# Kernel tuning notes

Measured on AMD Instinct MI355X. Metric: run time of the kernel, lower is better.

Reference implementation:

```python
import jax, jax.numpy as jnp
import numpy as np

B, S, H = 2, 2048, 2048
NH, NKV, HD = 16, 4, 128
ROPE_BASE = 10000.0


def setup_inputs() -> dict:
    key = jax.random.key(0)
    ks = jax.random.split(key, 5)
    x = jax.random.normal(ks[0], (B, S, H), dtype=jnp.float32)
    position_ids = jnp.arange(S, dtype=jnp.int64 if jax.config.jax_enable_x64 else jnp.int32).reshape(1, S)
    # Linear weights stored as [in, out] (equivalent to torch weight.T)
    sc = 1.0 / np.sqrt(H)
    Wq = jax.random.normal(ks[1], (H, NH * HD), dtype=jnp.float32) * sc
    Wk = jax.random.normal(ks[2], (H, NKV * HD), dtype=jnp.float32) * sc
    Wv = jax.random.normal(ks[3], (H, NKV * HD), dtype=jnp.float32) * sc
    Wo = jax.random.normal(ks[4], (NH * HD, H), dtype=jnp.float32) * (1.0 / np.sqrt(NH * HD))
    return {"x": x, "position_ids": position_ids, "Wq": Wq, "Wk": Wk, "Wv": Wv, "Wo": Wo}


def _rope(q, k, position_ids):
    # q: [B,S,NH,HD], k: [B,S,NKV,HD]; Llama-style half-split RoPE
    half = HD // 2
    inv_freq = 1.0 / (ROPE_BASE ** (jnp.arange(0, half, dtype=jnp.float32) * 2.0 / HD))
    ang = position_ids.astype(jnp.float32)[..., None] * inv_freq  # [b,S,half]
    cos = jnp.concatenate([jnp.cos(ang), jnp.cos(ang)], axis=-1)[:, :, None, :]  # [b,S,1,HD]
    sin = jnp.concatenate([jnp.sin(ang), jnp.sin(ang)], axis=-1)[:, :, None, :]

    def rot_half(t):
        t1, t2 = t[..., :half], t[..., half:]
        return jnp.concatenate([-t2, t1], axis=-1)

    return q * cos + rot_half(q) * sin, k * cos + rot_half(k) * sin


def reference(x, position_ids, Wq, Wk, Wv, Wo):
    b, s, _ = x.shape
    q = (x @ Wq).reshape(b, s, NH, HD)
    k = (x @ Wk).reshape(b, s, NKV, HD)
    v = (x @ Wv).reshape(b, s, NKV, HD)
    q, k = _rope(q, k, position_ids)
    reps = NH // NKV
    k = jnp.repeat(k, reps, axis=2)  # repeat_interleave on head dim
    v = jnp.repeat(v, reps, axis=2)
    q = q.transpose(0, 2, 1, 3)  # [b,h,s,d]
    k = k.transpose(0, 2, 1, 3)
    v = v.transpose(0, 2, 1, 3)
    scores = jnp.einsum('bhqd,bhkd->bhqk', q, k) / jnp.sqrt(jnp.float32(HD))
    causal = jnp.triu(jnp.ones((s, s), dtype=bool), k=1)
    scores = jnp.where(causal, -jnp.inf, scores)
    attn = jax.nn.softmax(scores.astype(jnp.float32), axis=-1).astype(q.dtype)
    out = jnp.einsum('bhqk,bhkd->bhqd', attn, v)
    out = out.transpose(0, 2, 1, 3).reshape(b, s, NH * HD)
    return out @ Wo
```

## Files before the change

kernel.cpp:

```cpp
#include <hip/hip_runtime.h>
#include <stdint.h>

typedef unsigned short u16;
typedef __attribute__((ext_vector_type(8))) short short8;
typedef __attribute__((ext_vector_type(4))) short short4v;
typedef __attribute__((ext_vector_type(4))) float floatx4;

#define S_LEN 2048
#define NQKV 3072

#if __has_builtin(__builtin_amdgcn_exp2f)
#define EXP2F __builtin_amdgcn_exp2f
#else
#define EXP2F exp2f
#endif

__device__ inline float bf2f(u16 u) {
  union { uint32_t u; float f; } v; v.u = ((uint32_t)u) << 16; return v.f;
}
__device__ inline u16 f2bf(float f) {
  union { float f; uint32_t u; } v; v.f = f;
  uint32_t r = v.u + 0x7fffu + ((v.u >> 16) & 1u);
  return (u16)(r >> 16);
}
__device__ inline void gl2lds16(const u16* g, u16* l) {
  __builtin_amdgcn_global_load_lds((const __attribute__((address_space(1))) uint32_t*)g,
                                   (__attribute__((address_space(3))) uint32_t*)l, 16, 0, 0);
}

__global__ void prep_k(const float* __restrict__ x, u16* __restrict__ Xb,
                       const float* __restrict__ Wq, const float* __restrict__ Wk,
                       const float* __restrict__ Wv, const float* __restrict__ Wo,
                       u16* __restrict__ WT, u16* __restrict__ WoT,
                       const int* __restrict__ pos, float2* __restrict__ rtab) {
  __shared__ u16 tile[64][33];
  const int b = blockIdx.x, t = threadIdx.x;
  if (b < 8192) {
    int i = b * 256 + t;
    float4 v = ((const float4*)x)[i];
    ushort4 o;
    o.x = f2bf(v.x); o.y = f2bf(v.y); o.z = f2bf(v.z); o.w = f2bf(v.w);
    ((ushort4*)Xb)[i] = o;
    return;
  }
  if (b >= 13312) {
    int i = (b - 13312) * 256 + t;
    int s = i >> 6, d = i & 63;
    float freq = __expf(-(float)d * 0.015625f * 9.210340371976184f);
    float ang = (float)pos[s] * freq;
    rtab[i] = make_float2(cosf(ang), sinf(ang));
    return;
  }
  int wb = b - 8192;
  const float* src; u16* dst; int bx, by, N;
  if (wb < 2048)      { src = Wq; dst = WT;                       bx = wb & 63;          by = wb >> 6;          N = 2048; }
  else if (wb < 2560) { src = Wk; dst = WT + (size_t)2048 * 2048; bx = (wb - 2048) & 15; by = (wb - 2048) >> 4; N = 512;  }
  else if (wb < 3072) { src = Wv; dst = WT + (size_t)2560 * 2048; bx = (wb - 2560) & 15; by = (wb - 2560) >> 4; N = 512;  }
  else                { src = Wo; dst = WoT;                      bx = (wb - 3072) & 63; by = (wb - 3072) >> 6; N = 2048; }
  int n0 = bx * 32, k0 = by * 64;
  int tx = t & 31, ty = t >> 5;
#pragma unroll
  for (int i = 0; i < 8; i++)
    tile[ty + 8 * i][tx] = f2bf(src[(size_t)(k0 + ty + 8 * i) * N + n0 + tx]);
  __syncthreads();
  int n = t >> 3, kc = (t & 7) * 8;
  short8 v;
#pragma unroll
  for (int j = 0; j < 8; j++) v[j] = (short)tile[kc + j][n];
  *(short8*)(dst + (size_t)(n0 + n) * 2048 + k0 + kc) = v;
}

__global__ __launch_bounds__(256) void gemm128_k(const u16* __restrict__ A,
                                                 const u16* __restrict__ Bt,
                                                 float* __restrict__ C, int M, int N, int K) {
  __shared__ u16 Al[2][8192];
  __shared__ u16 Bl[2][8192];
  const int TN = N >> 7;
  int flat = blockIdx.x;
  const int cpx = gridDim.x >> 3;
  flat = (flat & 7) * cpx + (flat >> 3);
  const int m0 = (flat / TN) << 7, n0 = (flat % TN) << 7;
  const int t = threadIdx.x, w = t >> 6, lane = t & 63;
  const int quad = lane >> 4, l16 = lane & 15;
  const int wm = w >> 1, wn = w & 1;
  const int sr = t >> 3, sl = t & 7;
  floatx4 acc[4][4] = {};
  const int NKT = K >> 6;
  const int ra_l = wm * 64 + l16;
  const int rb_l = wn * 64 + l16;

#pragma unroll
  for (int round = 0; round < 4; round++) {
    int r = round * 32 + sr;
    int so = (sl ^ (r & 7)) << 3;
    gl2lds16(A + (size_t)(m0 + r) * K + so, &Al[0][0] + round * 2048 + t * 8);
    gl2lds16(Bt + (size_t)(n0 + r) * K + so, &Bl[0][0] + round * 2048 + t * 8);
  }
  asm volatile("s_waitcnt vmcnt(0)" ::: "memory");
  __builtin_amdgcn_s_barrier();

  for (int kt = 0; kt < NKT; kt++) {
    const int cur = kt & 1;
    __builtin_amdgcn_s_barrier();
    if (kt + 1 < NKT) {
      const int k1 = (kt + 1) << 6;
#pragma unroll
      for (int round = 0; round < 4; round++) {
        int r = round * 32 + sr;
        int so = (sl ^ (r & 7)) << 3;
        gl2lds16(A + (size_t)(m0 + r) * K + k1 + so, &Al[cur ^ 1][0] + round * 2048 + t * 8);
        gl2lds16(Bt + (size_t)(n0 + r) * K + k1 + so, &Bl[cur ^ 1][0] + round * 2048 + t * 8);
      }
      asm volatile("s_waitcnt vmcnt(8)" ::: "memory");
    } else {
      asm volatile("s_waitcnt vmcnt(0)" ::: "memory");
    }
    __builtin_amdgcn_s_barrier();
    const u16* Ab = &Al[cur][0];
    const u16* Bb = &Bl[cur][0];
    short8 af[4][2], bf[4][2];
#pragma unroll
    for (int mt = 0; mt < 4; mt++) {
      int ra = ra_l + mt * 16;
      const u16* base = Ab + ra * 64;
#pragma unroll
      for (int ks = 0; ks < 2; ks++)
        af[mt][ks] = *(const short8*)(base + (((ks * 4 + quad) ^ (ra & 7)) << 3));
    }
#pragma unroll
    for (int nt = 0; nt < 4; nt++) {
      int rb = rb_l + nt * 16;
      const u16* base = Bb + rb * 64;
#pragma unroll
      for (int ks = 0; ks < 2; ks++)
        bf[nt][ks] = *(const short8*)(base + (((ks * 4 + quad) ^ (rb & 7)) << 3));
    }
    __builtin_amdgcn_s_setprio(1);
#pragma unroll
    for (int mt = 0; mt < 4; mt++)
#pragma unroll
      for (int nt = 0; nt < 4; nt++)
#pragma unroll
        for (int ks = 0; ks < 2; ks++)
          acc[mt][nt] = __builtin_amdgcn_mfma_f32_16x16x32_bf16(af[mt][ks], bf[nt][ks], acc[mt][nt], 0, 0, 0);
    __builtin_amdgcn_s_setprio(0);
  }
#pragma unroll
  for (int mt = 0; mt < 4; mt++)
#pragma unroll
    for (int nt = 0; nt < 4; nt++)
#pragma unroll
      for (int r = 0; r < 4; r++) {
        int row = m0 + wm * 64 + mt * 16 + quad * 4 + r;
        int col = n0 + wn * 64 + nt * 16 + l16;
        C[(size_t)row * N + col] = acc[mt][nt][r];
      }
}

__global__ __launch_bounds__(512, 2) void gemm256_k(const u16* __restrict__ A,
                                                    const u16* __restrict__ Bt,
                                                    u16* __restrict__ C,
                                                    const float2* __restrict__ rtab,
                                                    int N, int K) {
  __shared__ u16 SM[65536];
  u16* const AlB = SM;
  u16* const BlB = SM + 32768;
  const int TN = N >> 8;
  int flat = blockIdx.x;
  const int cpx = gridDim.x >> 3;
  flat = (flat & 7) * cpx + (flat >> 3);
  const int m0 = (flat / TN) << 8, n0 = (flat % TN) << 8;
  const int t = threadIdx.x, w = t >> 6, lane = t & 63;
  const int quad = lane >> 4, l16 = lane & 15;
  const int wm = w >> 2, wn = w & 3;
  const int sr = t >> 3, sl = t & 7;
  floatx4 acc[2][2][4][2] = {};
  const int NKT = K >> 6;

  const int ra_l = wm * 64 + l16;
  const int rb_l = wn * 16 + l16;

#pragma unroll
  for (int round = 0; round < 2; round++) {
    int r = round * 64 + sr;
    int so = (sl ^ (r & 7)) << 3;
    gl2lds16(A + (size_t)(m0 + r) * K + so, AlB + round * 4096 + t * 8);
    gl2lds16(Bt + (size_t)(n0 + r) * K + so, BlB + round * 4096 + t * 8);
    gl2lds16(Bt + (size_t)(n0 + 128 + r) * K + so, BlB + 8192 + round * 4096 + t * 8);
    gl2lds16(A + (size_t)(m0 + 128 + r) * K + so, AlB + 8192 + round * 4096 + t * 8);
  }
  asm volatile("s_waitcnt vmcnt(0)" ::: "memory");
  __builtin_amdgcn_s_barrier();

  short8 af[4][2];
  short8 bf[2][2][2];

  for (int kt = 0; kt < NKT; kt++) {
    const int c = kt & 1;
    const u16* Ab = AlB + c * 16384;
    const u16* Bb = BlB + c * 16384;
    u16* An = AlB + (c ^ 1) * 16384;
    u16* Bn = BlB + (c ^ 1) * 16384;
    const int k1 = (kt + 1) << 6;
    const bool pf = (kt + 1 < NKT);
#pragma unroll
    for (int ph = 0; ph < 4; ph++) {
      const int mh = (ph >> 1);
      const int nh = (ph == 1 || ph == 2) ? 1 : 0;
      if (ph == 0 || ph == 1) {
#pragma unroll
        for (int nt = 0; nt < 2; nt++) {
          int rb = rb_l + nt * 64;
          const u16* base = Bb + nh * 8192 + rb * 64;
#pragma unroll
          for (int ks = 0; ks < 2; ks++)
            bf[nh][nt][ks] = *(const short8*)(base + (((ks * 4 + quad) ^ (rb & 7)) << 3));
        }
      }
      if (ph == 0 || ph == 2) {
#pragma unroll
        for (int mt = 0; mt < 4; mt++) {
          int ra = ra_l + mt * 16;
          const u16* base = Ab + mh * 8192 + ra * 64;
#pragma unroll
          for (int ks = 0; ks < 2; ks++)
            af[mt][ks] = *(const short8*)(base + (((ks * 4 + quad) ^ (ra & 7)) << 3));
        }
      }
      if (pf) {
        const u16* G;
        u16* L;
        int rbase;
        if (ph == 0)      { G = A;  L = An;        rbase = m0; }
        else if (ph == 1) { G = Bt; L = Bn;        rbase = n0; }
        else if (ph == 2) { G = Bt; L = Bn + 8192; rbase = n0 + 128; }
        else              { G = A;  L = An + 8192; rbase = m0 + 128; }
#pragma unroll
        for (int round = 0; round < 2; round++) {
          int r = round * 64 + sr;
          gl2lds16(G + (size_t)(rbase + r) * K + k1 + ((sl ^ (r & 7)) << 3),
                   L + round * 4096 + t * 8);
        }
      }
      __builtin_amdgcn_s_barrier();
      __builtin_amdgcn_s_setprio(1);
#pragma unroll
      for (int mt = 0; mt < 4; mt++)
#pragma unroll
        for (int nt = 0; nt < 2; nt++)
#pragma unroll
          for (int ks = 0; ks < 2; ks++)
            acc[mh][nh][mt][nt] =
                __builtin_amdgcn_mfma_f32_16x16x32_bf16(af[mt][ks], bf[nh][nt][ks], acc[mh][nh][mt][nt], 0, 0, 0);
      __builtin_amdgcn_s_setprio(0);
      if (ph != 2) {
        if (pf) asm volatile("s_waitcnt vmcnt(4)" ::: "memory");
        else    asm volatile("s_waitcnt vmcnt(0)" ::: "memory");
      }
      __builtin_amdgcn_s_barrier();
    }
  }
  if (n0 < 2560) {
    const int dloc = wn * 16 + l16;
#pragma unroll
    for (int mh = 0; mh < 2; mh++)
#pragma unroll
      for (int mt = 0; mt < 4; mt++)
#pragma unroll
        for (int r = 0; r < 4; r++) {
          int row = m0 + mh * 128 + wm * 64 + mt * 16 + quad * 4 + r;
          float2 cs = rtab[(row & (S_LEN - 1)) * 64 + dloc];
#pragma unroll
          for (int nh = 0; nh < 2; nh++) {
            float a0 = acc[mh][nh][mt][0][r], a1 = acc[mh][nh][mt][1][r];
            float o0 = a0 * cs.x - a1 * cs.y;
            float o1 = a1 * cs.x + a0 * cs.y;
            int colb = n0 + nh * 128 + wn * 16 + l16;
            C[(size_t)row * N + colb]      = f2bf(o0);
            C[(size_t)row * N + colb + 64] = f2bf(o1);
          }
        }
  } else {
    const int bbv = m0 >> 11, m0loc = m0 & 2047;
    const int kvbase = (n0 - 2560) >> 7;
#pragma unroll
    for (int mh = 0; mh < 2; mh++)
#pragma unroll
      for (int nh = 0; nh < 2; nh++)
#pragma unroll
        for (int mt = 0; mt < 4; mt++)
#pragma unroll
          for (int pair = 0; pair < 2; pair++) {
            int lrow = mh * 128 + wm * 64 + mt * 16 + quad * 4;
            int lcol = nh * 128 + wn * 16 + l16 + pair * 64;
            short4v v4 = { (short)f2bf(acc[mh][nh][mt][pair][0]),
                           (short)f2bf(acc[mh][nh][mt][pair][1]),
                           (short)f2bf(acc[mh][nh][mt][pair][2]),
                           (short)f2bf(acc[mh][nh][mt][pair][3]) };
            *(short4v*)(SM + lcol * 256 + (lrow ^ ((lcol & 15) << 3))) = v4;
          }
    asm volatile("s_waitcnt lgkmcnt(0)" ::: "memory");
    __builtin_amdgcn_s_barrier();
#pragma unroll
    for (int it = 0; it < 16; it++) {
      int u = it * 512 + t;
      int key0 = (u & 31) * 8, lcol = u >> 5;
      short8 v = *(const short8*)(SM + lcol * 256 + (key0 ^ ((lcol & 15) << 3)));
      int d = lcol & 127, kvh = kvbase + (lcol >> 7);
      int key = m0loc + key0;
      *(short8*)(C + (size_t)(bbv * 2048 + kvh * 512 + d * 4 + (key >> 9)) * N + 2560 + (key & 511)) = v;
    }
  }
}

__global__ __launch_bounds__(256) void attn_k(const u16* __restrict__ qkv,
                                              u16* __restrict__ ctx) {
  __shared__ u16 Kl[2][64 * 128];
  __shared__ u16 Vl[2][128 * 64];
  const int f = blockIdx.x;
  const int p = f >> 5;
  const int hb = f & 31;
  const int h = hb & 15, bb = hb >> 4;
  const int kvh = h >> 2;
  const int t = threadIdx.x, w = t >> 6, lane = t & 63;
  const int quad = lane >> 4, l16 = lane & 15;
  const int sx = l16 & 7;
  const int kslot = lane & 15;
  const int vd0 = w * 32 + (lane >> 3);
  const int vslot = lane & 7;
  const int grow0 = (w & 1) * 4 + (w >> 1) * 32 + quad;
  const size_t rowbase = (size_t)bb * S_LEN;
  const u16* Kg0 = qkv + rowbase * NQKV + 2048 + kvh * 128;
  const u16* Vg0 = qkv + (rowbase + kvh * 512) * NQKV + 2560;
  const float c2 = 0.12751744f;
  short8 onesf = {16256, 16256, 16256, 16256, 16256, 16256, 16256, 16256};

  for (int phase = 0; phase < 2; phase++) {
    const int qt = phase ? p : 31 - p;
    const int rw = qt * 64 + w * 16;
    const int qrow = rw + l16;

    short8 qf[4];
#pragma unroll
    for (int ks = 0; ks < 4; ks++)
      qf[ks] = *(const short8*)(qkv + (rowbase + rw + l16) * NQKV + h * 128 + ks * 32 + quad * 8);

    floatx4 acc[8] = {};
    floatx4 accl = {0.f, 0.f, 0.f, 0.f};

    __syncthreads();
    {
#pragma unroll
      for (int ii = 0; ii < 4; ii++) {
        int p7 = (quad + 4 * ii) & 7;
        int grow = grow0 + 8 * ii;
        gl2lds16(Kg0 + (size_t)grow * NQKV + ((kslot ^ p7) * 8),
                 &Kl[0][0] + w * 2048 + ii * 512 + lane * 8);
      }
#pragma unroll
      for (int ii = 0; ii < 4; ii++) {
        int d = vd0 + ii * 8;
        int s8 = (vslot ^ (d & 7)) * 8;
        gl2lds16(Vg0 + (size_t)(d * 4) * NQKV + s8,
                 &Vl[0][0] + w * 2048 + ii * 512 + lane * 8);
      }
    }

    for (int kb = 0; kb <= qt; kb++) {
      const int cur = kb & 1;
      __builtin_amdgcn_s_barrier();
      if (kb < qt) {
        const int kn = kb + 1;
        const u16* Kg = Kg0 + (size_t)kn * 64 * NQKV;
        u16* KlN = &Kl[cur ^ 1][0];
        u16* VlN = &Vl[cur ^ 1][0];
#pragma unroll
        for (int ii = 0; ii < 4; ii++) {
          int p7 = (quad + 4 * ii) & 7;
          int grow = grow0 + 8 * ii;
          gl2lds16(Kg + (size_t)grow * NQKV + ((kslot ^ p7) * 8),
                   KlN + w * 2048 + ii * 512 + lane * 8);
        }
#pragma unroll
        for (int ii = 0; ii < 4; ii++) {
          int d = vd0 + ii * 8;
          int s8 = (vslot ^ (d & 7)) * 8;
          gl2lds16(Vg0 + (size_t)(d * 4 + (kn >> 3)) * NQKV + (kn & 7) * 64 + s8,
                   VlN + w * 2048 + ii * 512 + lane * 8);
        }
        asm volatile("s_waitcnt vmcnt(8)" ::: "memory");
      } else {
        asm volatile("s_waitcnt vmcnt(0)" ::: "memory");
      }
      __builtin_amdgcn_s_barrier();
      const u16* KlB = &Kl[cur][0];
      const u16* VlB = &Vl[cur][0];

      floatx4 sc[4];
      __builtin_amdgcn_s_setprio(1);
#pragma unroll
      for (int nt = 0; nt < 4; nt++) {
        const u16* Krow = KlB + (nt * 16 + l16) * 128;
        short8 kf[4];
#pragma unroll
        for (int ks = 0; ks < 4; ks++)
          kf[ks] = *(const short8*)(Krow + (((ks * 4 + quad) ^ sx) * 8));
        floatx4 s = {0.f, 0.f, 0.f, 0.f};
#pragma unroll
        for (int ks = 0; ks < 4; ks++) s = __builtin_amdgcn_mfma_f32_16x16x32_bf16(kf[ks], qf[ks], s, 0, 0, 0);
        sc[nt] = s;
      }
      __builtin_amdgcn_s_setprio(0);
      const bool diag = (kb == qt);
      uint32_t pw[8];
#pragma unroll
      for (int nt = 0; nt < 4; nt++) {
        uint32_t w0 = 0, w1 = 0;
#pragma unroll
        for (int r = 0; r < 4; r++) {
          float e = EXP2F(sc[nt][r] * c2);
          if (diag) {
            int keyg = kb * 64 + quad * 8 + (nt & 1) * 4 + (nt >> 1) * 32 + r;
            if (keyg > qrow) e = 0.f;
          }
          uint32_t b = __float_as_uint(e) >> 16;
          if (r == 0) w0 = b;
          else if (r == 1) w0 |= b << 16;
          else if (r == 2) w1 = b;
          else w1 |= b << 16;
        }
        pw[nt * 2] = w0;
        pw[nt * 2 + 1] = w1;
      }
      union { short8 v; uint32_t u[4]; } pu0, pu1;
      pu0.u[0] = pw[0]; pu0.u[1] = pw[1]; pu0.u[2] = pw[2]; pu0.u[3] = pw[3];
      pu1.u[0] = pw[4]; pu1.u[1] = pw[5]; pu1.u[2] = pw[6]; pu1.u[3] = pw[7];
      const short8 pf0 = pu0.v, pf1 = pu1.v;

      __builtin_amdgcn_s_setprio(1);
      accl = __builtin_amdgcn_mfma_f32_16x16x32_bf16(pf0, onesf, accl, 0, 0, 0);
      accl = __builtin_amdgcn_mfma_f32_16x16x32_bf16(pf1, onesf, accl, 0, 0, 0);
#pragma unroll
      for (int nto = 0; nto < 8; nto++) {
        const u16* Vrow = VlB + (nto * 16 + l16) * 64;
        short8 vf0 = *(const short8*)(Vrow + ((quad ^ sx) * 8));
        short8 vf1 = *(const short8*)(Vrow + (((quad + 4) ^ sx) * 8));
        acc[nto] = __builtin_amdgcn_mfma_f32_16x16x32_bf16(pf0, vf0, acc[nto], 0, 0, 0);
        acc[nto] = __builtin_amdgcn_mfma_f32_16x16x32_bf16(pf1, vf1, acc[nto], 0, 0, 0);
      }
      __builtin_amdgcn_s_setprio(0);
    }
#pragma unroll
    for (int r = 0; r < 4; r++) {
      float inv = 1.0f / accl[r];
      int rowg = rw + quad * 4 + r;
#pragma unroll
      for (int nto = 0; nto < 8; nto++) {
        int col = h * 128 + nto * 16 + l16;
        ctx[(rowbase + rowg) * 2048 + col] = f2bf(acc[nto][r] * inv);
      }
    }
  }
}

extern "C" void kernel_launch(void* const* d_in, const int* in_sizes, int n_in,
                              void* d_out, int out_size, void* d_ws, size_t ws_size,
                              hipStream_t stream) {
  const float* x  = (const float*)d_in[0];
  const int* pos  = (const int*)d_in[1];
  const float* Wq = (const float*)d_in[2];
  const float* Wk = (const float*)d_in[3];
  const float* Wv = (const float*)d_in[4];
  const float* Wo = (const float*)d_in[5];
  float* out = (float*)d_out;
  char* ws = (char*)d_ws;
  u16* Xb  = (u16*)(ws);
  u16* WT  = (u16*)(ws + 16777216);
  u16* WoT = (u16*)(ws + 29360128);
  u16* QKV = (u16*)(ws + 37748736);
  u16* CTX = (u16*)(ws + 62914560);
  float2* rtab = (float2*)(ws + 62914560);

  hipLaunchKernelGGL(prep_k, dim3(13824), dim3(256), 0, stream, x, Xb, Wq, Wk, Wv, Wo, WT, WoT, pos, rtab);

  hipLaunchKernelGGL(gemm256_k, dim3(192), dim3(512), 0, stream, Xb, WT, QKV, rtab, 3072, 2048);
  hipLaunchKernelGGL(attn_k, dim3(512), dim3(256), 0, stream, QKV, CTX);
  hipLaunchKernelGGL(gemm128_k, dim3(512), dim3(256), 0, stream, CTX, WoT, out, 4096, 2048, 2048);
}
```

Measured before the change: 269.5 us.

## Replace four-phase interleaved GEMM k-loop with single-barrier prefetch-all schedule

Restructures the QKV GEMM main loop. It now issues all next-tile global-to-LDS loads at the start of each k-iteration, runs all four MFMA quadrants from LDS fragments without intermediate barriers, and waits on vmcnt(0) with a single barrier at the end. This removes the per-phase barriers and partial waitcnts, cutting synchronisation overhead. In exchange the load issue is burstier and there is less fine-grained overlap of memory traffic with compute.

Result: no change. 264.6 us (-1.8%).

```diff
diff --git a/kernel.cpp b/kernel.cpp
--- a/kernel.cpp
+++ b/kernel.cpp
@@ -201,64 +201,86 @@
     const u16* Bb = BlB + c * 16384;
     u16* An = AlB + (c ^ 1) * 16384;
     u16* Bn = BlB + (c ^ 1) * 16384;
-    const int k1 = (kt + 1) << 6;
-    const bool pf = (kt + 1 < NKT);
-#pragma unroll
-    for (int ph = 0; ph < 4; ph++) {
-      const int mh = (ph >> 1);
-      const int nh = (ph == 1 || ph == 2) ? 1 : 0;
-      if (ph == 0 || ph == 1) {
-#pragma unroll
-        for (int nt = 0; nt < 2; nt++) {
-          int rb = rb_l + nt * 64;
-          const u16* base = Bb + nh * 8192 + rb * 64;
-#pragma unroll
-          for (int ks = 0; ks < 2; ks++)
-            bf[nh][nt][ks] = *(const short8*)(base + (((ks * 4 + quad) ^ (rb & 7)) << 3));
-        }
-      }
-      if (ph == 0 || ph == 2) {
-#pragma unroll
-        for (int mt = 0; mt < 4; mt++) {
-          int ra = ra_l + mt * 16;
-          const u16* base = Ab + mh * 8192 + ra * 64;
-#pragma unroll
-          for (int ks = 0; ks < 2; ks++)
-            af[mt][ks] = *(const short8*)(base + (((ks * 4 + quad) ^ (ra & 7)) << 3));
-        }
-      }
-      if (pf) {
-        const u16* G;
-        u16* L;
-        int rbase;
-        if (ph == 0)      { G = A;  L = An;        rbase = m0; }
-        else if (ph == 1) { G = Bt; L = Bn;        rbase = n0; }
-        else if (ph == 2) { G = Bt; L = Bn + 8192; rbase = n0 + 128; }
-        else              { G = A;  L = An + 8192; rbase = m0 + 128; }
-#pragma unroll
-        for (int round = 0; round < 2; round++) {
-          int r = round * 64 + sr;
-          gl2lds16(G + (size_t)(rbase + r) * K + k1 + ((sl ^ (r & 7)) << 3),
-                   L + round * 4096 + t * 8);
-        }
-      }
-      __builtin_amdgcn_s_barrier();
-      __builtin_amdgcn_s_setprio(1);
-#pragma unroll
-      for (int mt = 0; mt < 4; mt++)
-#pragma unroll
-        for (int nt = 0; nt < 2; nt++)
-#pragma unroll
-          for (int ks = 0; ks < 2; ks++)
-            acc[mh][nh][mt][nt] =
-                __builtin_amdgcn_mfma_f32_16x16x32_bf16(af[mt][ks], bf[nh][nt][ks], acc[mh][nh][mt][nt], 0, 0, 0);
-      __builtin_amdgcn_s_setprio(0);
-      if (ph != 2) {
-        if (pf) asm volatile("s_waitcnt vmcnt(4)" ::: "memory");
-        else    asm volatile("s_waitcnt vmcnt(0)" ::: "memory");
-      }
-      __builtin_amdgcn_s_barrier();
-    }
+    if (kt + 1 < NKT) {
+      const int k1 = (kt + 1) << 6;
+#pragma unroll
+      for (int round = 0; round < 2; round++) {
+        int r = round * 64 + sr;
+        int so = (sl ^ (r & 7)) << 3;
+        gl2lds16(A + (size_t)(m0 + r) * K + k1 + so, An + round * 4096 + t * 8);
+        gl2lds16(Bt + (size_t)(n0 + r) * K + k1 + so, Bn + round * 4096 + t * 8);
+        gl2lds16(Bt + (size_t)(n0 + 128 + r) * K + k1 + so, Bn + 8192 + round * 4096 + t * 8);
+        gl2lds16(A + (size_t)(m0 + 128 + r) * K + k1 + so, An + 8192 + round * 4096 + t * 8);
+      }
+    }
+    __builtin_amdgcn_s_setprio(1);
+#pragma unroll
+    for (int nt = 0; nt < 2; nt++) {
+      int rb = rb_l + nt * 64;
+      const u16* base = Bb + rb * 64;
+#pragma unroll
+      for (int ks = 0; ks < 2; ks++)
+        bf[0][nt][ks] = *(const short8*)(base + (((ks * 4 + quad) ^ (rb & 7)) << 3));
+    }
+#pragma unroll
+    for (int mt = 0; mt < 4; mt++) {
+      int ra = ra_l + mt * 16;
+      const u16* base = Ab + ra * 64;
+#pragma unroll
+      for (int ks = 0; ks < 2; ks++)
+        af[mt][ks] = *(const short8*)(base + (((ks * 4 + quad) ^ (ra & 7)) << 3));
+    }
+#pragma unroll
+    for (int mt = 0; mt < 4; mt++)
+#pragma unroll
+      for (int nt = 0; nt < 2; nt++)
+#pragma unroll
+        for (int ks = 0; ks < 2; ks++)
+          acc[0][0][mt][nt] =
+              __builtin_amdgcn_mfma_f32_16x16x32_bf16(af[mt][ks], bf[0][nt][ks], acc[0][0][mt][nt], 0, 0, 0);
+#pragma unroll
+    for (int nt = 0; nt < 2; nt++) {
+      int rb = rb_l + nt * 64;
+      const u16* base = Bb + 8192 + rb * 64;
+#pragma unroll
+      for (int ks = 0; ks < 2; ks++)
+        bf[1][nt][ks] = *(const short8*)(base + (((ks * 4 + quad) ^ (rb & 7)) << 3));
+    }
+#pragma unroll
+    for (int mt = 0; mt < 4; mt++)
+#pragma unroll
+      for (int nt = 0; nt < 2; nt++)
+#pragma unroll
+        for (int ks = 0; ks < 2; ks++)
+          acc[0][1][mt][nt] =
+              __builtin_amdgcn_mfma_f32_16x16x32_bf16(af[mt][ks], bf[1][nt][ks], acc[0][1][mt][nt], 0, 0, 0);
+#pragma unroll
+    for (int mt = 0; mt < 4; mt++) {
+      int ra = ra_l + mt * 16;
+      const u16* base = Ab + 8192 + ra * 64;
+#pragma unroll
+      for (int ks = 0; ks < 2; ks++)
+        af[mt][ks] = *(const short8*)(base + (((ks * 4 + quad) ^ (ra & 7)) << 3));
+    }
+#pragma unroll
+    for (int mt = 0; mt < 4; mt++)
+#pragma unroll
+      for (int nt = 0; nt < 2; nt++)
+#pragma unroll
+        for (int ks = 0; ks < 2; ks++)
+          acc[1][1][mt][nt] =
+              __builtin_amdgcn_mfma_f32_16x16x32_bf16(af[mt][ks], bf[1][nt][ks], acc[1][1][mt][nt], 0, 0, 0);
+#pragma unroll
+    for (int mt = 0; mt < 4; mt++)
+#pragma unroll
+      for (int nt = 0; nt < 2; nt++)
+#pragma unroll
+        for (int ks = 0; ks < 2; ks++)
+          acc[1][0][mt][nt] =
+              __builtin_amdgcn_mfma_f32_16x16x32_bf16(af[mt][ks], bf[0][nt][ks], acc[1][0][mt][nt], 0, 0, 0);
+    __builtin_amdgcn_s_setprio(0);
+    asm volatile("s_waitcnt vmcnt(0)" ::: "memory");
+    __builtin_amdgcn_s_barrier();
   }
   if (n0 < 2560) {
     const int dloc = wn * 16 + l16;
```
